# Optimization experiments

Hardware: AMD Instinct MI355X
Metric: run time of the kernel (lower is better)

## Reference

```python
import jax, jax.numpy as jnp
import numpy as np

N = 10000          # nodes
E = 80000          # edges
STATE_DIM = 18
HID = 1024
LAYERS = 4


def setup_inputs() -> dict:
    key = jax.random.key(0)
    ks = jax.random.split(key, 16)
    s = 0.02
    x = jax.random.normal(ks[0], (N, STATE_DIM), dtype=jnp.float32)
    edge_index = jax.random.randint(ks[1], (2, E), 0, N, dtype=jnp.int32)
    # frozen inverse-phase embedding projection (no bias)
    proj_w = jax.random.normal(ks[2], (STATE_DIM, HID), dtype=jnp.float32) * s
    # per-layer message MLP: Linear(2*HID -> HID) -> ReLU -> Linear(HID -> HID)
    W1 = jax.random.normal(ks[3], (LAYERS, 2 * HID, HID), dtype=jnp.float32) * s
    b1 = jnp.zeros((LAYERS, HID), dtype=jnp.float32)
    W2 = jax.random.normal(ks[4], (LAYERS, HID, HID), dtype=jnp.float32) * s
    b2 = jnp.zeros((LAYERS, HID), dtype=jnp.float32)
    # ghost head: Linear(HID->256) -> ReLU -> Linear(256->1) -> Sigmoid
    gw1 = jax.random.normal(ks[5], (HID, 256), dtype=jnp.float32) * s
    gb1 = jnp.zeros((256,), dtype=jnp.float32)
    gw2 = jax.random.normal(ks[6], (256, 1), dtype=jnp.float32) * s
    gb2 = jnp.zeros((1,), dtype=jnp.float32)
    # state head: Linear(HID -> STATE_DIM)
    sw = jax.random.normal(ks[7], (HID, STATE_DIM), dtype=jnp.float32) * s
    sb = jnp.zeros((STATE_DIM,), dtype=jnp.float32)
    return {"x": x, "edge_index": edge_index, "proj_w": proj_w,
            "W1": W1, "b1": b1, "W2": W2, "b2": b2,
            "gw1": gw1, "gb1": gb1, "gw2": gw2, "gb2": gb2,
            "sw": sw, "sb": sb}


def reference(x, edge_index, proj_w, W1, b1, W2, b2, gw1, gb1, gw2, gb2, sw, sb):
    src = edge_index[0]  # j (source)
    dst = edge_index[1]  # i (target), aggr='add' scatters into i
    # InversePhaseEmbedding: sin(h)*cos(h)
    p = x @ proj_w                      # [N, HID]
    h = jnp.sin(p) * jnp.cos(p)
    for l in range(LAYERS):
        x_i = h[dst]                    # [E, HID] gather target feats
        x_j = h[src]                    # [E, HID] gather source feats
        msg = jnp.concatenate([x_i, x_j - x_i], axis=-1)  # [E, 2*HID]
        m = jax.nn.relu(msg @ W1[l] + b1[l]) @ W2[l] + b2[l]  # [E, HID]
        h = jax.ops.segment_sum(m, dst, num_segments=N)       # scatter-add
        h = jax.nn.relu(h)
    ghost_score = jax.nn.sigmoid(jax.nn.relu(h @ gw1 + gb1) @ gw2 + gb2)  # [N,1]
    stable_state = h @ sw + sb                                            # [N,18]
    return ghost_score, stable_state, h
```

## Files before the change

kernel.cpp:

```cpp
#include <hip/hip_runtime.h>
#include <hip/hip_bf16.h>
#include <math.h>

#define NN 10000
#define EE 80000
#define SDIM 18
#define HID 1024
#define NLAYERS 4
#define GHID 256

typedef __bf16 bf16;
typedef __bf16 bf16x8 __attribute__((ext_vector_type(8)));
typedef __bf16 bf16x4 __attribute__((ext_vector_type(4)));
typedef float f32x4 __attribute__((ext_vector_type(4)));

#define AS1C(p) ((const __attribute__((address_space(1))) void*)(p))
#define AS3(p)  ((__attribute__((address_space(3))) void*)(p))

__global__ void zeroi_kernel(int* __restrict__ p, int n) {
    int i = blockIdx.x * 256 + threadIdx.x;
    if (i < n) p[i] = 0;
}

__global__ void count_kernel(const int* __restrict__ ei, int* __restrict__ cnt) {
    int e = blockIdx.x * 256 + threadIdx.x;
    if (e < EE) atomicAdd(&cnt[ei[EE + e]], 1);
}

__global__ __launch_bounds__(256) void scan_kernel(const int* __restrict__ cnt,
                                                   int* __restrict__ offs,
                                                   int* __restrict__ cursor,
                                                   float* __restrict__ degF) {
    const int CH = 40;
    __shared__ int partial[256];
    int t = threadIdx.x;
    int base = t * CH;
    int local[CH];
    int sum = 0;
#pragma unroll
    for (int i = 0; i < CH; ++i) {
        int idx = base + i;
        int v = (idx < NN) ? cnt[idx] : 0;
        local[i] = sum;
        sum += v;
    }
    partial[t] = sum;
    __syncthreads();
    for (int off = 1; off < 256; off <<= 1) {
        int v = (t >= off) ? partial[t - off] : 0;
        __syncthreads();
        partial[t] += v;
        __syncthreads();
    }
    int excl = (t == 0) ? 0 : partial[t - 1];
#pragma unroll
    for (int i = 0; i < CH; ++i) {
        int idx = base + i;
        if (idx < NN) {
            int o = excl + local[i];
            offs[idx] = o;
            cursor[idx] = o;
            degF[idx] = (float)cnt[idx];
        }
    }
    if (t == 255) offs[NN] = partial[255];
}

__global__ void scatter_kernel(const int* __restrict__ ei, int* __restrict__ cursor,
                               int* __restrict__ esrc) {
    int e = blockIdx.x * 256 + threadIdx.x;
    if (e < EE) {
        int dst = ei[EE + e];
        int pos = atomicAdd(&cursor[dst], 1);
        esrc[pos] = ei[e];
    }
}

__global__ __launch_bounds__(256) void tconvW1_kernel(const float* __restrict__ W1,
                                                      bf16* __restrict__ WT) {
    __shared__ float td[32][33];
    __shared__ float tb[32][33];
    const size_t H2 = (size_t)HID * HID;
    const float* s = W1 + (size_t)blockIdx.z * 2 * H2;
    bf16* d = WT + (size_t)blockIdx.z * 2 * H2;
    int bx = blockIdx.x * 32;
    int by = blockIdx.y * 32;
    int tx = threadIdx.x, ty = threadIdx.y;
#pragma unroll
    for (int r = 0; r < 4; ++r) {
        int row = by + ty + r * 8;
        float vt = s[(size_t)row * HID + bx + tx];
        float vb = s[H2 + (size_t)row * HID + bx + tx];
        td[ty + r * 8][tx] = vt - vb;
        tb[ty + r * 8][tx] = vb;
    }
    __syncthreads();
#pragma unroll
    for (int r = 0; r < 4; ++r) {
        int orow = bx + ty + r * 8;
        d[(size_t)orow * HID + by + tx] = (bf16)td[tx][ty + r * 8];
        d[(size_t)(HID + orow) * HID + by + tx] = (bf16)tb[tx][ty + r * 8];
    }
}

__global__ __launch_bounds__(256) void tconv_kernel(const float* __restrict__ src, long sstride,
                                                    bf16* __restrict__ dst, long dstride,
                                                    int M, int N) {
    __shared__ float t[32][33];
    const float* s = src + (size_t)blockIdx.z * sstride;
    bf16* d = dst + (size_t)blockIdx.z * dstride;
    int bx = blockIdx.x * 32;
    int by = blockIdx.y * 32;
    int tx = threadIdx.x, ty = threadIdx.y;
#pragma unroll
    for (int r = 0; r < 4; ++r) {
        int row = by + ty + r * 8;
        t[ty + r * 8][tx] = s[(size_t)row * N + bx + tx];
    }
    __syncthreads();
#pragma unroll
    for (int r = 0; r < 4; ++r) {
        int orow = bx + ty + r * 8;
        d[(size_t)orow * M + by + tx] = (bf16)t[tx][ty + r * 8];
    }
}

__global__ void swt_kernel(const float* __restrict__ sw, bf16* __restrict__ swt) {
    int i = blockIdx.x * 256 + threadIdx.x;
    int n = i >> 10, k = i & 1023;
    swt[i] = (bf16)(n < SDIM ? sw[k * SDIM + n] : 0.f);
}

__global__ void bias2_kernel(const float* __restrict__ b1, float* __restrict__ cb) {
    int i = blockIdx.x * 256 + threadIdx.x;
    int l = i >> 11, c = i & 2047;
    cb[i] = (c < HID) ? b1[l * HID + c] : 0.f;
}

__global__ __launch_bounds__(256) void proj_kernel(const float* __restrict__ x,
                                                   const float* __restrict__ pw,
                                                   bf16* __restrict__ hb) {
    int row = blockIdx.y;
    int col = blockIdx.x * 256 + threadIdx.x;
    __shared__ float xr[SDIM];
    if (threadIdx.x < SDIM) xr[threadIdx.x] = x[row * SDIM + threadIdx.x];
    __syncthreads();
    float acc = 0.f;
#pragma unroll
    for (int k = 0; k < SDIM; ++k) acc += xr[k] * pw[k * HID + col];
    hb[(size_t)row * HID + col] = (bf16)(sinf(acc) * cosf(acc));
}

template <int RELU, int HAS_BIAS, int HAS_RS, int WF32, int WB16>
__global__ __launch_bounds__(256) void mgemm_kernel(const bf16* __restrict__ A,
                                                    const bf16* __restrict__ Bt,
                                                    float* __restrict__ C,
                                                    bf16* __restrict__ Cb,
                                                    const float* __restrict__ bias,
                                                    const float* __restrict__ rowscale,
                                                    int M, int N, int K) {
    __shared__ bf16 As[128 * 32];
    __shared__ bf16 Bs[128 * 32];
    const int tid = threadIdx.x;
    const int m0 = blockIdx.y * 128;
    const int n0 = blockIdx.x * 128;
    const int wave = tid >> 6;
    const int wr = (wave >> 1) * 64, wc = (wave & 1) * 64;
    const int lane = tid & 63;
    const int quad = lane >> 4, r15 = lane & 15;

    f32x4 acc[4][4] = {};

    const int s0 = tid, s1 = 256 + tid;
    int ar0 = m0 + (s0 >> 2); ar0 = ar0 < M ? ar0 : M - 1;
    int ar1 = m0 + (s1 >> 2); ar1 = ar1 < M ? ar1 : M - 1;
    const bf16* ga0 = A + (size_t)ar0 * K + (s0 & 3) * 8;
    const bf16* ga1 = A + (size_t)ar1 * K + (s1 & 3) * 8;
    const bf16* gb0 = Bt + (size_t)(n0 + (s0 >> 2)) * K + (s0 & 3) * 8;
    const bf16* gb1 = Bt + (size_t)(n0 + (s1 >> 2)) * K + (s1 & 3) * 8;
    bf16* lA0 = As + (size_t)(tid & ~63) * 8;
    bf16* lA1 = As + (size_t)(256 + (tid & ~63)) * 8;
    bf16* lB0 = Bs + (size_t)(tid & ~63) * 8;
    bf16* lB1 = Bs + (size_t)(256 + (tid & ~63)) * 8;

    for (int k0 = 0; k0 < K; k0 += 32) {
        __syncthreads();
        __builtin_amdgcn_global_load_lds(AS1C(ga0 + k0), AS3(lA0), 16, 0, 0);
        __builtin_amdgcn_global_load_lds(AS1C(ga1 + k0), AS3(lA1), 16, 0, 0);
        __builtin_amdgcn_global_load_lds(AS1C(gb0 + k0), AS3(lB0), 16, 0, 0);
        __builtin_amdgcn_global_load_lds(AS1C(gb1 + k0), AS3(lB1), 16, 0, 0);
        __syncthreads();
        bf16x8 af[4], bfr[4];
#pragma unroll
        for (int i = 0; i < 4; ++i)
            af[i] = *(const bf16x8*)(As + (wr + i * 16 + r15) * 32 + quad * 8);
#pragma unroll
        for (int j = 0; j < 4; ++j)
            bfr[j] = *(const bf16x8*)(Bs + (wc + j * 16 + r15) * 32 + quad * 8);
#pragma unroll
        for (int i = 0; i < 4; ++i)
#pragma unroll
            for (int j = 0; j < 4; ++j)
                acc[i][j] = __builtin_amdgcn_mfma_f32_16x16x32_bf16(af[i], bfr[j], acc[i][j], 0, 0, 0);
    }

#pragma unroll
    for (int i = 0; i < 4; ++i) {
#pragma unroll
        for (int r = 0; r < 4; ++r) {
            int grow = m0 + wr + i * 16 + quad * 4 + r;
            if (grow >= M) continue;
            float rs = HAS_RS ? rowscale[grow] : 1.f;
#pragma unroll
            for (int j = 0; j < 4; ++j) {
                int gcol = n0 + wc + j * 16 + r15;
                float v = acc[i][j][r];
                if (HAS_BIAS) v += rs * bias[gcol];
                if (RELU) v = fmaxf(v, 0.f);
                if (WF32) C[(size_t)grow * N + gcol] = v;
                if (WB16) Cb[(size_t)grow * N + gcol] = (bf16)v;
            }
        }
    }
}

__global__ __launch_bounds__(256) void gather_kernel(const int* __restrict__ offs,
                                                     const int* __restrict__ esrc,
                                                     const bf16* __restrict__ CB,
                                                     bf16* __restrict__ Sb) {
    int node = blockIdx.x;
    int c = threadIdx.x * 4;
    int k0 = offs[node], k1 = offs[node + 1];
    bf16x4 cv = *(const bf16x4*)(CB + (size_t)node * 2048 + c);
    float cx = (float)cv.x, cy = (float)cv.y, cz = (float)cv.z, cw = (float)cv.w;
    float ax = 0.f, ay = 0.f, az = 0.f, aw = 0.f;
    for (int k = k0; k < k1; ++k) {
        int s = esrc[k];
        bf16x4 bv = *(const bf16x4*)(CB + (size_t)s * 2048 + 1024 + c);
        ax += fmaxf(cx + (float)bv.x, 0.f);
        ay += fmaxf(cy + (float)bv.y, 0.f);
        az += fmaxf(cz + (float)bv.z, 0.f);
        aw += fmaxf(cw + (float)bv.w, 0.f);
    }
    bf16x4 o;
    o.x = (bf16)ax; o.y = (bf16)ay; o.z = (bf16)az; o.w = (bf16)aw;
    *(bf16x4*)(Sb + (size_t)node * HID + c) = o;
}

__global__ __launch_bounds__(64) void stable_mfma_kernel(const bf16* __restrict__ hb,
                                                         const bf16* __restrict__ swt,
                                                         const float* __restrict__ sb,
                                                         float* __restrict__ out) {
    int m0 = blockIdx.x * 16;
    int lane = threadIdx.x;
    int quad = lane >> 4, r15 = lane & 15;
    f32x4 acc0 = {}, acc1 = {};
    const bf16* arow = hb + (size_t)(m0 + r15) * HID + quad * 8;
    const bf16* b0 = swt + (size_t)r15 * HID + quad * 8;
    const bf16* b1p = swt + (size_t)(16 + r15) * HID + quad * 8;
    for (int k0 = 0; k0 < HID; k0 += 32) {
        bf16x8 af = *(const bf16x8*)(arow + k0);
        bf16x8 bf0 = *(const bf16x8*)(b0 + k0);
        bf16x8 bf1 = *(const bf16x8*)(b1p + k0);
        acc0 = __builtin_amdgcn_mfma_f32_16x16x32_bf16(af, bf0, acc0, 0, 0, 0);
        acc1 = __builtin_amdgcn_mfma_f32_16x16x32_bf16(af, bf1, acc1, 0, 0, 0);
    }
#pragma unroll
    for (int r = 0; r < 4; ++r) {
        int grow = m0 + quad * 4 + r;
        out[(size_t)grow * SDIM + r15] = acc0[r] + sb[r15];
        if (r15 < 2) out[(size_t)grow * SDIM + 16 + r15] = acc1[r] + sb[16 + r15];
    }
}

__global__ __launch_bounds__(256) void ghost_kernel(const float* __restrict__ g1,
                                                    const float* __restrict__ gw2,
                                                    const float* __restrict__ gb2,
                                                    float* __restrict__ out) {
    int row = blockIdx.x;
    int t = threadIdx.x;
    float v = g1[(size_t)row * GHID + t] * gw2[t];
#pragma unroll
    for (int o = 32; o > 0; o >>= 1) v += __shfl_down(v, o, 64);
    __shared__ float red[4];
    if ((t & 63) == 0) red[t >> 6] = v;
    __syncthreads();
    if (t == 0) {
        float s = red[0] + red[1] + red[2] + red[3] + gb2[0];
        out[row] = 1.f / (1.f + expf(-s));
    }
}

extern "C" void kernel_launch(void* const* d_in, const int* in_sizes, int n_in,
                              void* d_out, int out_size, void* d_ws, size_t ws_size,
                              hipStream_t stream) {
    const float* x   = (const float*)d_in[0];
    const int*   ei  = (const int*)d_in[1];
    const float* pw  = (const float*)d_in[2];
    const float* W1  = (const float*)d_in[3];
    const float* b1  = (const float*)d_in[4];
    const float* W2  = (const float*)d_in[5];
    const float* b2  = (const float*)d_in[6];
    const float* gw1 = (const float*)d_in[7];
    const float* gb1 = (const float*)d_in[8];
    const float* gw2 = (const float*)d_in[9];
    const float* gb2 = (const float*)d_in[10];
    const float* sw  = (const float*)d_in[11];
    const float* sb  = (const float*)d_in[12];

    float* out    = (float*)d_out;
    float* ghost  = out;
    float* stable = out + NN;
    float* h      = out + NN + NN * SDIM;

    const size_t H2 = (size_t)HID * HID;
    float* ws   = (float*)d_ws;
    float* g1   = ws;
    float* degF = g1 + (size_t)NN * GHID;
    float* cb   = degF + NN;
    bf16* hb    = (bf16*)(cb + 4 * 2048);
    bf16* Sb    = hb + (size_t)NN * HID;
    bf16* CB    = Sb + (size_t)NN * HID;
    bf16* WT    = CB + (size_t)NN * 2048;
    bf16* W2t   = WT + 8 * H2;
    bf16* gw1t  = W2t + 4 * H2;
    bf16* swt   = gw1t + (size_t)GHID * HID;
    int*  cnt    = (int*)(swt + 32 * 1024);
    int*  offs   = cnt + NN;
    int*  cursor = offs + NN + 1;
    int*  esrc   = cursor + NN;

    zeroi_kernel<<<dim3((NN + 255) / 256), 256, 0, stream>>>(cnt, NN);
    count_kernel<<<dim3((EE + 255) / 256), 256, 0, stream>>>(ei, cnt);
    scan_kernel<<<dim3(1), 256, 0, stream>>>(cnt, offs, cursor, degF);
    scatter_kernel<<<dim3((EE + 255) / 256), 256, 0, stream>>>(ei, cursor, esrc);

    dim3 tb(32, 8);
    tconvW1_kernel<<<dim3(32, 32, 4), tb, 0, stream>>>(W1, WT);
    tconv_kernel<<<dim3(32, 32, 4), tb, 0, stream>>>(W2, (long)H2, W2t, (long)H2, HID, HID);
    tconv_kernel<<<dim3(GHID / 32, HID / 32, 1), tb, 0, stream>>>(gw1, 0, gw1t, 0, HID, GHID);
    swt_kernel<<<dim3(32 * 1024 / 256), 256, 0, stream>>>(sw, swt);
    bias2_kernel<<<dim3(4 * 2048 / 256), 256, 0, stream>>>(b1, cb);

    proj_kernel<<<dim3(HID / 256, NN), 256, 0, stream>>>(x, pw, hb);

    dim3 gfused(2048 / 128, (NN + 127) / 128);
    dim3 gw2g(HID / 128, (NN + 127) / 128);
    for (int l = 0; l < NLAYERS; ++l) {
        mgemm_kernel<0, 1, 0, 0, 1><<<gfused, 256, 0, stream>>>(
            hb, WT + (size_t)l * 2 * H2, nullptr, CB, cb + l * 2048, nullptr, NN, 2048, HID);
        gather_kernel<<<dim3(NN), 256, 0, stream>>>(offs, esrc, CB, Sb);
        if (l < NLAYERS - 1)
            mgemm_kernel<1, 1, 1, 0, 1><<<gw2g, 256, 0, stream>>>(
                Sb, W2t + (size_t)l * H2, nullptr, hb, b2 + (size_t)l * HID, degF, NN, HID, HID);
        else
            mgemm_kernel<1, 1, 1, 1, 1><<<gw2g, 256, 0, stream>>>(
                Sb, W2t + (size_t)l * H2, h, hb, b2 + (size_t)l * HID, degF, NN, HID, HID);
    }

    mgemm_kernel<1, 1, 0, 1, 0><<<dim3(GHID / 128, (NN + 127) / 128), 256, 0, stream>>>(
        hb, gw1t, g1, nullptr, gb1, nullptr, NN, GHID, HID);
    ghost_kernel<<<dim3(NN), 256, 0, stream>>>(g1, gw2, gb2, ghost);
    stable_mfma_kernel<<<dim3(NN / 16), 64, 0, stream>>>(hb, swt, sb, stable);
}
```

Baseline: 810.7 us.

## Use k-plane LDS layout with padding and grouped block swizzle in GEMM

The GEMM's shared-memory tiles are rearranged from row-major [128][32] into four k-slice planes of 128x8 elements, each padded to 1032 elements. Each wave loads one plane chunk directly into LDS, and MFMA fragment reads become contiguous 16-byte reads per lane within a plane. The intent is to avoid LDS bank conflicts on the fragment reads. Block indices are also remapped into groups of eight M-tiles so that concurrently running blocks share A and B tiles in L2, at the cost of a little index arithmetic.

```diff
diff --git a/kernel.cpp b/kernel.cpp
--- a/kernel.cpp
+++ b/kernel.cpp
@@ -16,6 +16,8 @@
 
 #define AS1C(p) ((const __attribute__((address_space(1))) void*)(p))
 #define AS3(p)  ((__attribute__((address_space(3))) void*)(p))
+
+#define PLANE_ELEMS 1032
 
 __global__ void zeroi_kernel(int* __restrict__ p, int n) {
     int i = blockIdx.x * 256 + threadIdx.x;
@@ -159,11 +161,23 @@
                                                     const float* __restrict__ bias,
                                                     const float* __restrict__ rowscale,
                                                     int M, int N, int K) {
-    __shared__ bf16 As[128 * 32];
-    __shared__ bf16 Bs[128 * 32];
+    __shared__ __align__(16) bf16 As[4 * PLANE_ELEMS];
+    __shared__ __align__(16) bf16 Bs[4 * PLANE_ELEMS];
     const int tid = threadIdx.x;
-    const int m0 = blockIdx.y * 128;
-    const int n0 = blockIdx.x * 128;
+
+    const int num_n = gridDim.x, num_m = gridDim.y;
+    int bid = blockIdx.x + blockIdx.y * num_n;
+    const int GROUP = 8;
+    int width = GROUP * num_n;
+    int group = bid / width;
+    int rem = bid - group * width;
+    int rows_ing = num_m - group * GROUP;
+    rows_ing = rows_ing < GROUP ? rows_ing : GROUP;
+    int by = group * GROUP + rem % rows_ing;
+    int bx = rem / rows_ing;
+    const int m0 = by * 128;
+    const int n0 = bx * 128;
+
     const int wave = tid >> 6;
     const int wr = (wave >> 1) * 64, wc = (wave & 1) * 64;
     const int lane = tid & 63;
@@ -171,32 +185,34 @@
 
     f32x4 acc[4][4] = {};
 
-    const int s0 = tid, s1 = 256 + tid;
-    int ar0 = m0 + (s0 >> 2); ar0 = ar0 < M ? ar0 : M - 1;
-    int ar1 = m0 + (s1 >> 2); ar1 = ar1 < M ? ar1 : M - 1;
-    const bf16* ga0 = A + (size_t)ar0 * K + (s0 & 3) * 8;
-    const bf16* ga1 = A + (size_t)ar1 * K + (s1 & 3) * 8;
-    const bf16* gb0 = Bt + (size_t)(n0 + (s0 >> 2)) * K + (s0 & 3) * 8;
-    const bf16* gb1 = Bt + (size_t)(n0 + (s1 >> 2)) * K + (s1 & 3) * 8;
-    bf16* lA0 = As + (size_t)(tid & ~63) * 8;
-    bf16* lA1 = As + (size_t)(256 + (tid & ~63)) * 8;
-    bf16* lB0 = Bs + (size_t)(tid & ~63) * 8;
-    bf16* lB1 = Bs + (size_t)(256 + (tid & ~63)) * 8;
+    const int rA = (wave & 1) * 64 + lane;
+    const int ks1 = wave >> 1;
+    const int ks2 = 2 + (wave >> 1);
+    int grA = m0 + rA; grA = grA < M ? grA : M - 1;
+    const int grB = n0 + rA;
+    const bf16* gA1 = A + (size_t)grA * K + ks1 * 8;
+    const bf16* gA2 = A + (size_t)grA * K + ks2 * 8;
+    const bf16* gB1 = Bt + (size_t)grB * K + ks1 * 8;
+    const bf16* gB2 = Bt + (size_t)grB * K + ks2 * 8;
+    bf16* lA1 = As + ks1 * PLANE_ELEMS + (wave & 1) * 512;
+    bf16* lA2 = As + ks2 * PLANE_ELEMS + (wave & 1) * 512;
+    bf16* lB1 = Bs + ks1 * PLANE_ELEMS + (wave & 1) * 512;
+    bf16* lB2 = Bs + ks2 * PLANE_ELEMS + (wave & 1) * 512;
 
     for (int k0 = 0; k0 < K; k0 += 32) {
         __syncthreads();
-        __builtin_amdgcn_global_load_lds(AS1C(ga0 + k0), AS3(lA0), 16, 0, 0);
-        __builtin_amdgcn_global_load_lds(AS1C(ga1 + k0), AS3(lA1), 16, 0, 0);
-        __builtin_amdgcn_global_load_lds(AS1C(gb0 + k0), AS3(lB0), 16, 0, 0);
-        __builtin_amdgcn_global_load_lds(AS1C(gb1 + k0), AS3(lB1), 16, 0, 0);
+        __builtin_amdgcn_global_load_lds(AS1C(gA1 + k0), AS3(lA1), 16, 0, 0);
+        __builtin_amdgcn_global_load_lds(AS1C(gA2 + k0), AS3(lA2), 16, 0, 0);
+        __builtin_amdgcn_global_load_lds(AS1C(gB1 + k0), AS3(lB1), 16, 0, 0);
+        __builtin_amdgcn_global_load_lds(AS1C(gB2 + k0), AS3(lB2), 16, 0, 0);
         __syncthreads();
         bf16x8 af[4], bfr[4];
 #pragma unroll
         for (int i = 0; i < 4; ++i)
-            af[i] = *(const bf16x8*)(As + (wr + i * 16 + r15) * 32 + quad * 8);
+            af[i] = *(const bf16x8*)(As + quad * PLANE_ELEMS + (wr + i * 16 + r15) * 8);
 #pragma unroll
         for (int j = 0; j < 4; ++j)
-            bfr[j] = *(const bf16x8*)(Bs + (wc + j * 16 + r15) * 32 + quad * 8);
+            bfr[j] = *(const bf16x8*)(Bs + quad * PLANE_ELEMS + (wc + j * 16 + r15) * 8);
 #pragma unroll
         for (int i = 0; i < 4; ++i)
 #pragma unroll
```

New measurement: 965.9 us. 1.19x slower.
